# Optimization experiments

Hardware: AMD Instinct MI355X
Metric: run time of the kernel (lower is better)

Reference implementation:

```python
import jax, jax.numpy as jnp
import numpy as np

B, N, L, ND = 512, 4096, 128, 1


def setup_inputs() -> dict:
    key = jax.random.key(0)
    ks = jax.random.split(key, 20)
    g = lambda k, shape, s=0.05: jax.random.normal(k, shape, dtype=jnp.float32) * s
    IN = 3 * L + ND  # MLP input: [mem, mem, delta_t, x]
    inp = {
        "x": jax.random.normal(ks[0], (B, N, ND), jnp.float32),
        "memory": jax.random.normal(ks[1], (N, L), jnp.float32),
        "delta_t": jax.random.normal(ks[2], (B, N, L), jnp.float32),
        "src_w1": g(ks[3], (L, IN)), "src_b1": g(ks[4], (L,)),
        "src_w2": g(ks[5], (L, L)), "src_b2": g(ks[6], (L,)),
        "tar_w1": g(ks[7], (L, IN)), "tar_b1": g(ks[8], (L,)),
        "tar_w2": g(ks[9], (L, L)), "tar_b2": g(ks[10], (L,)),
        "gru_wih": g(ks[11], (3 * L, L)), "gru_whh": g(ks[12], (3 * L, L)),
        "gru_bih": g(ks[13], (3 * L,)), "gru_bhh": g(ks[14], (3 * L,)),
        "source": jax.random.randint(ks[15], (B, 1), 0, N, dtype=jnp.int64),
        "target": jax.random.randint(ks[16], (B, 1), 0, N, dtype=jnp.int64),
    }
    return inp


def _mlp(h, w1, b1, w2, b2):
    return jax.nn.relu(h @ w1.T + b1) @ w2.T + b2


def _gru_cell(inp, h, wih, whh, bih, bhh):
    gi = inp @ wih.T + bih          # [n, 3L]
    gh = h @ whh.T + bhh            # [n, 3L]
    i_r, i_z, i_n = jnp.split(gi, 3, axis=-1)
    h_r, h_z, h_n = jnp.split(gh, 3, axis=-1)
    r = jax.nn.sigmoid(i_r + h_r)
    z = jax.nn.sigmoid(i_z + h_z)
    n = jnp.tanh(i_n + r * h_n)
    return (1.0 - z) * n + z * h


def reference(x, memory, delta_t, src_w1, src_b1, src_w2, src_b2,
              tar_w1, tar_b1, tar_w2, tar_b2,
              gru_wih, gru_whh, gru_bih, gru_bhh, source, target):
    b = x.shape[0]
    bi = jnp.arange(b)
    s = source[:, 0]
    t = target[:, 0]
    src_mem = memory[s]                 # [B, L]
    tar_mem = memory[t]                 # [B, L]
    src_x = x[bi, s, :]                 # [B, ND]
    tar_x = x[bi, t, :]
    src_dt = delta_t[bi, s, :]          # [B, L]
    tar_dt = delta_t[bi, t, :]
    src_in = jnp.concatenate([src_mem, tar_mem, src_dt, src_x], axis=-1)
    tar_in = jnp.concatenate([tar_mem, src_mem, tar_dt, tar_x], axis=-1)
    src_msg = _mlp(src_in, src_w1, src_b1, src_w2, src_b2)
    tar_msg = _mlp(tar_in, tar_w1, tar_b1, tar_w2, tar_b2)

    # unique + scatter_mean == segment-mean over node ids, touching only seen nodes
    ids = jnp.concatenate([s, t], axis=0)                       # [2B]
    msgs = jnp.concatenate([src_msg, tar_msg], axis=0)          # [2B, L]
    n_nodes = memory.shape[0]
    msg_sum = jax.ops.segment_sum(msgs, ids, num_segments=n_nodes)
    cnt = jax.ops.segment_sum(jnp.ones((ids.shape[0],), msgs.dtype), ids,
                              num_segments=n_nodes)
    agg = msg_sum / jnp.maximum(cnt, 1.0)[:, None]              # [N, L]
    new_mem = _gru_cell(agg, memory, gru_wih, gru_whh, gru_bih, gru_bhh)
    seen = (cnt > 0)[:, None]
    return jnp.where(seen, new_mem, memory)
```

## Files before the change

kernel.cpp:

```cpp
#include <hip/hip_runtime.h>
#include <math.h>

#define BB 512
#define NN 4096
#define LL 128
#define IN_DIM 385
#define NK4_1 97
#define NK4_2 32
#define EPB 2
#define GPB 4

#define OFF_MSG   0
#define OFF_CNT   (OFF_MSG + NN * LL)
#define OFF_COUNT (OFF_CNT + NN)
#define OFF_LIST  (OFF_COUNT + 4)
#define OFF_W1PS  529416
#define OFF_W1PT  (OFF_W1PS + NK4_1 * LL * 4)
#define OFF_W2PS  (OFF_W1PT + NK4_1 * LL * 4)
#define OFF_W2PT  (OFF_W2PS + NK4_2 * LL * 4)
#define OFF_WIHP  (OFF_W2PT + NK4_2 * LL * 4)
#define OFF_WHHP  (OFF_WIHP + 3 * NK4_2 * LL * 4)

__global__ __launch_bounds__(256) void prep_kernel(
    const float* __restrict__ sw1, const float* __restrict__ tw1,
    const float* __restrict__ sw2, const float* __restrict__ tw2,
    const float* __restrict__ wih, const float* __restrict__ whh,
    float* __restrict__ ws)
{
    const int i = blockIdx.x * 256 + threadIdx.x;
    const int stride = gridDim.x * 256;

    float4* msg4 = (float4*)(ws + OFF_MSG);
    const float4 z4 = make_float4(0.f, 0.f, 0.f, 0.f);
    for (int idx = i; idx < NN * LL / 4; idx += stride)
        msg4[idx] = z4;
    for (int idx = i; idx < NN; idx += stride)
        ws[OFF_CNT + idx] = 0.0f;
    if (i == 0)
        ((int*)ws)[OFF_COUNT] = 0;

    float4* w1ps = (float4*)(ws + OFF_W1PS);
    float4* w1pt = (float4*)(ws + OFF_W1PT);
    for (int idx = i; idx < NK4_1 * LL; idx += stride) {
        const int k4 = idx >> 7, j = idx & 127;
        const int k = k4 * 4;
        float4 a, b;
        a.x = sw1[j * IN_DIM + k];     b.x = tw1[j * IN_DIM + k];
        a.y = (k + 1 < IN_DIM) ? sw1[j * IN_DIM + k + 1] : 0.f;
        b.y = (k + 1 < IN_DIM) ? tw1[j * IN_DIM + k + 1] : 0.f;
        a.z = (k + 2 < IN_DIM) ? sw1[j * IN_DIM + k + 2] : 0.f;
        b.z = (k + 2 < IN_DIM) ? tw1[j * IN_DIM + k + 2] : 0.f;
        a.w = (k + 3 < IN_DIM) ? sw1[j * IN_DIM + k + 3] : 0.f;
        b.w = (k + 3 < IN_DIM) ? tw1[j * IN_DIM + k + 3] : 0.f;
        w1ps[idx] = a; w1pt[idx] = b;
    }
    float4* w2ps = (float4*)(ws + OFF_W2PS);
    float4* w2pt = (float4*)(ws + OFF_W2PT);
    for (int idx = i; idx < NK4_2 * LL; idx += stride) {
        const int k4 = idx >> 7, j = idx & 127;
        const int k = k4 * 4;
        w2ps[idx] = make_float4(sw2[j * LL + k], sw2[j * LL + k + 1],
                                sw2[j * LL + k + 2], sw2[j * LL + k + 3]);
        w2pt[idx] = make_float4(tw2[j * LL + k], tw2[j * LL + k + 1],
                                tw2[j * LL + k + 2], tw2[j * LL + k + 3]);
    }
    float4* wihp = (float4*)(ws + OFF_WIHP);
    float4* whhp = (float4*)(ws + OFF_WHHP);
    for (int idx = i; idx < 3 * NK4_2 * LL; idx += stride) {
        const int j = idx & 127;
        const int gk = idx >> 7;
        const int gate = gk >> 5, k4 = gk & 31;
        const int row = gate * LL + j, k = k4 * 4;
        wihp[idx] = make_float4(wih[row * LL + k], wih[row * LL + k + 1],
                                wih[row * LL + k + 2], wih[row * LL + k + 3]);
        whhp[idx] = make_float4(whh[row * LL + k], whh[row * LL + k + 1],
                                whh[row * LL + k + 2], whh[row * LL + k + 3]);
    }
}

__global__ __launch_bounds__(256) void edge_msg_kernel(
    const float* __restrict__ x,
    const float* __restrict__ memory,
    const float* __restrict__ delta_t,
    const float* __restrict__ sb1, const float* __restrict__ sb2,
    const float* __restrict__ tb1, const float* __restrict__ tb2,
    const int* __restrict__ source, const int* __restrict__ target,
    float* __restrict__ ws, float* __restrict__ out)
{
    const int tid = threadIdx.x;

    if (blockIdx.x >= 512) {
        const int cb = blockIdx.x - 512;
        float4* out4 = (float4*)out;
        const float4* mem4 = (const float4*)memory;
        for (int idx = cb * 256 + tid; idx < NN * LL / 4; idx += 32 * 256)
            out4[idx] = mem4[idx];
        return;
    }

    const int side  = blockIdx.x & 1;
    const int chunk = blockIdx.x >> 1;
    const int g     = tid >> 7;
    const int j     = tid & 127;

    const int eg0 = chunk * EPB, eg1 = eg0 + 1;
    const int s0 = source[eg0], t0 = target[eg0];
    const int s1 = source[eg1], t1 = target[eg1];
    const int node0  = side ? t0 : s0, other0 = side ? s0 : t0;
    const int node1  = side ? t1 : s1, other1 = side ? s1 : t1;

    __shared__ float h1[LL][EPB];
    __shared__ float part1[2][EPB][LL];
    __shared__ float part2[2][EPB][LL];

    const float4* w1p = (const float4*)(ws + (side ? OFF_W1PT : OFF_W1PS));
    const float4* w2p = (const float4*)(ws + (side ? OFF_W2PT : OFF_W2PS));
    const float* b1  = side ? tb1 : sb1;
    const float* b2  = side ? tb2 : sb2;

    {
        float a0 = 0.f, a1 = 0.f;
        const float* dA = delta_t + ((size_t)eg0 * NN + node0) * LL;
        const float* dB = delta_t + ((size_t)eg1 * NN + node1) * LL;
        if (g == 0) {
            const float* pA = memory + (size_t)node0 * LL;
            const float* pB = memory + (size_t)node1 * LL;
            #pragma unroll 4
            for (int k4 = 0; k4 < 32; ++k4) {
                const float4 w  = w1p[k4 * LL + j];
                const float4 iA = *(const float4*)(pA + 4 * k4);
                const float4 iB = *(const float4*)(pB + 4 * k4);
                a0 = fmaf(w.x, iA.x, a0); a1 = fmaf(w.x, iB.x, a1);
                a0 = fmaf(w.y, iA.y, a0); a1 = fmaf(w.y, iB.y, a1);
                a0 = fmaf(w.z, iA.z, a0); a1 = fmaf(w.z, iB.z, a1);
                a0 = fmaf(w.w, iA.w, a0); a1 = fmaf(w.w, iB.w, a1);
            }
            #pragma unroll 4
            for (int k4 = 64; k4 < 80; ++k4) {
                const float4 w  = w1p[k4 * LL + j];
                const float4 iA = *(const float4*)(dA + 4 * (k4 - 64));
                const float4 iB = *(const float4*)(dB + 4 * (k4 - 64));
                a0 = fmaf(w.x, iA.x, a0); a1 = fmaf(w.x, iB.x, a1);
                a0 = fmaf(w.y, iA.y, a0); a1 = fmaf(w.y, iB.y, a1);
                a0 = fmaf(w.z, iA.z, a0); a1 = fmaf(w.z, iB.z, a1);
                a0 = fmaf(w.w, iA.w, a0); a1 = fmaf(w.w, iB.w, a1);
            }
        } else {
            const float* pA = memory + (size_t)other0 * LL;
            const float* pB = memory + (size_t)other1 * LL;
            #pragma unroll 4
            for (int k4 = 32; k4 < 64; ++k4) {
                const float4 w  = w1p[k4 * LL + j];
                const float4 iA = *(const float4*)(pA + 4 * (k4 - 32));
                const float4 iB = *(const float4*)(pB + 4 * (k4 - 32));
                a0 = fmaf(w.x, iA.x, a0); a1 = fmaf(w.x, iB.x, a1);
                a0 = fmaf(w.y, iA.y, a0); a1 = fmaf(w.y, iB.y, a1);
                a0 = fmaf(w.z, iA.z, a0); a1 = fmaf(w.z, iB.z, a1);
                a0 = fmaf(w.w, iA.w, a0); a1 = fmaf(w.w, iB.w, a1);
            }
            #pragma unroll 4
            for (int k4 = 80; k4 < 96; ++k4) {
                const float4 w  = w1p[k4 * LL + j];
                const float4 iA = *(const float4*)(dA + 4 * (k4 - 64));
                const float4 iB = *(const float4*)(dB + 4 * (k4 - 64));
                a0 = fmaf(w.x, iA.x, a0); a1 = fmaf(w.x, iB.x, a1);
                a0 = fmaf(w.y, iA.y, a0); a1 = fmaf(w.y, iB.y, a1);
                a0 = fmaf(w.z, iA.z, a0); a1 = fmaf(w.z, iB.z, a1);
                a0 = fmaf(w.w, iA.w, a0); a1 = fmaf(w.w, iB.w, a1);
            }
            {
                const float4 w = w1p[96 * LL + j];
                const float xA = x[(size_t)eg0 * NN + node0];
                const float xB = x[(size_t)eg1 * NN + node1];
                a0 = fmaf(w.x, xA, a0);
                a1 = fmaf(w.x, xB, a1);
            }
        }
        part1[g][0][j] = a0;
        part1[g][1][j] = a1;
    }
    __syncthreads();

    h1[j][g] = fmaxf(part1[0][g][j] + part1[1][g][j] + b1[j], 0.0f);
    __syncthreads();

    {
        const int k40 = g * 16, k41 = k40 + 16;
        float a0 = 0.f, a1 = 0.f;
        #pragma unroll 4
        for (int k4 = k40; k4 < k41; ++k4) {
            const float4 w  = w2p[k4 * LL + j];
            const float4 h0 = *(const float4*)&h1[k4 * 4][0];
            const float4 h2 = *(const float4*)&h1[k4 * 4 + 2][0];
            a0 = fmaf(w.x, h0.x, a0); a1 = fmaf(w.x, h0.y, a1);
            a0 = fmaf(w.y, h0.z, a0); a1 = fmaf(w.y, h0.w, a1);
            a0 = fmaf(w.z, h2.x, a0); a1 = fmaf(w.z, h2.y, a1);
            a0 = fmaf(w.w, h2.z, a0); a1 = fmaf(w.w, h2.w, a1);
        }
        part2[g][0][j] = a0;
        part2[g][1][j] = a1;
    }
    __syncthreads();

    {
        const int node = g ? node1 : node0;
        const float m = part2[0][g][j] + part2[1][g][j] + b2[j];
        atomicAdd(ws + OFF_MSG + (size_t)node * LL + j, m);
    }
    if (tid < EPB) {
        const int node = tid ? node1 : node0;
        const float old = atomicAdd(ws + OFF_CNT + node, 1.0f);
        if (old == 0.0f) {
            const int pos = atomicAdd((int*)ws + OFF_COUNT, 1);
            ((int*)ws)[OFF_LIST + pos] = node;
        }
    }
}

__global__ __launch_bounds__(256) void gru_kernel(
    const float* __restrict__ memory,
    const float* __restrict__ bih, const float* __restrict__ bhh,
    const float* __restrict__ ws,
    float* __restrict__ out)
{
    const int tid = threadIdx.x;
    const int g = tid >> 7, j = tid & 127;
    const int scount = ((const int*)ws)[OFF_COUNT];
    const int base = blockIdx.x * GPB;
    if (base >= scount) return;
    const int nact = min(GPB, scount - base);

    __shared__ float gates[6][GPB][LL];
    __shared__ int   nodes_sh[GPB];

    int nd[GPB];
    #pragma unroll
    for (int s = 0; s < GPB; ++s)
        nd[s] = (base + s < scount) ? ((const int*)ws)[OFF_LIST + base + s]
                                    : ((const int*)ws)[OFF_LIST + base];
    if (tid < GPB) nodes_sh[tid] = nd[tid];

    const float* op0; const float* op1; const float* op2; const float* op3;
    float rc0 = 1.f, rc1 = 1.f, rc2 = 1.f, rc3 = 1.f;
    if (g == 0) {
        op0 = ws + OFF_MSG + (size_t)nd[0] * LL;
        op1 = ws + OFF_MSG + (size_t)nd[1] * LL;
        op2 = ws + OFF_MSG + (size_t)nd[2] * LL;
        op3 = ws + OFF_MSG + (size_t)nd[3] * LL;
        rc0 = 1.0f / ws[OFF_CNT + nd[0]];
        rc1 = 1.0f / ws[OFF_CNT + nd[1]];
        rc2 = 1.0f / ws[OFF_CNT + nd[2]];
        rc3 = 1.0f / ws[OFF_CNT + nd[3]];
    } else {
        op0 = memory + (size_t)nd[0] * LL;
        op1 = memory + (size_t)nd[1] * LL;
        op2 = memory + (size_t)nd[2] * LL;
        op3 = memory + (size_t)nd[3] * LL;
    }

    const float4* wp = (const float4*)(ws + (g ? OFF_WHHP : OFF_WIHP));
    float a0[GPB] = {}, a1[GPB] = {}, a2[GPB] = {};
    #pragma unroll 2
    for (int k4 = 0; k4 < NK4_2; ++k4) {
        const float4 w0 = wp[(0 * NK4_2 + k4) * LL + j];
        const float4 w1 = wp[(1 * NK4_2 + k4) * LL + j];
        const float4 w2 = wp[(2 * NK4_2 + k4) * LL + j];
        const float4 v0 = *(const float4*)(op0 + 4 * k4);
        const float4 v1 = *(const float4*)(op1 + 4 * k4);
        const float4 v2 = *(const float4*)(op2 + 4 * k4);
        const float4 v3 = *(const float4*)(op3 + 4 * k4);
        a0[0] = fmaf(w0.x, v0.x, a0[0]); a0[0] = fmaf(w0.y, v0.y, a0[0]);
        a0[0] = fmaf(w0.z, v0.z, a0[0]); a0[0] = fmaf(w0.w, v0.w, a0[0]);
        a1[0] = fmaf(w1.x, v0.x, a1[0]); a1[0] = fmaf(w1.y, v0.y, a1[0]);
        a1[0] = fmaf(w1.z, v0.z, a1[0]); a1[0] = fmaf(w1.w, v0.w, a1[0]);
        a2[0] = fmaf(w2.x, v0.x, a2[0]); a2[0] = fmaf(w2.y, v0.y, a2[0]);
        a2[0] = fmaf(w2.z, v0.z, a2[0]); a2[0] = fmaf(w2.w, v0.w, a2[0]);

        a0[1] = fmaf(w0.x, v1.x, a0[1]); a0[1] = fmaf(w0.y, v1.y, a0[1]);
        a0[1] = fmaf(w0.z, v1.z, a0[1]); a0[1] = fmaf(w0.w, v1.w, a0[1]);
        a1[1] = fmaf(w1.x, v1.x, a1[1]); a1[1] = fmaf(w1.y, v1.y, a1[1]);
        a1[1] = fmaf(w1.z, v1.z, a1[1]); a1[1] = fmaf(w1.w, v1.w, a1[1]);
        a2[1] = fmaf(w2.x, v1.x, a2[1]); a2[1] = fmaf(w2.y, v1.y, a2[1]);
        a2[1] = fmaf(w2.z, v1.z, a2[1]); a2[1] = fmaf(w2.w, v1.w, a2[1]);

        a0[2] = fmaf(w0.x, v2.x, a0[2]); a0[2] = fmaf(w0.y, v2.y, a0[2]);
        a0[2] = fmaf(w0.z, v2.z, a0[2]); a0[2] = fmaf(w0.w, v2.w, a0[2]);
        a1[2] = fmaf(w1.x, v2.x, a1[2]); a1[2] = fmaf(w1.y, v2.y, a1[2]);
        a1[2] = fmaf(w1.z, v2.z, a1[2]); a1[2] = fmaf(w1.w, v2.w, a1[2]);
        a2[2] = fmaf(w2.x, v2.x, a2[2]); a2[2] = fmaf(w2.y, v2.y, a2[2]);
        a2[2] = fmaf(w2.z, v2.z, a2[2]); a2[2] = fmaf(w2.w, v2.w, a2[2]);

        a0[3] = fmaf(w0.x, v3.x, a0[3]); a0[3] = fmaf(w0.y, v3.y, a0[3]);
        a0[3] = fmaf(w0.z, v3.z, a0[3]); a0[3] = fmaf(w0.w, v3.w, a0[3]);
        a1[3] = fmaf(w1.x, v3.x, a1[3]); a1[3] = fmaf(w1.y, v3.y, a1[3]);
        a1[3] = fmaf(w1.z, v3.z, a1[3]); a1[3] = fmaf(w1.w, v3.w, a1[3]);
        a2[3] = fmaf(w2.x, v3.x, a2[3]); a2[3] = fmaf(w2.y, v3.y, a2[3]);
        a2[3] = fmaf(w2.z, v3.z, a2[3]); a2[3] = fmaf(w2.w, v3.w, a2[3]);
    }
    if (g == 0) {
        a0[0] *= rc0; a1[0] *= rc0; a2[0] *= rc0;
        a0[1] *= rc1; a1[1] *= rc1; a2[1] *= rc1;
        a0[2] *= rc2; a1[2] *= rc2; a2[2] *= rc2;
        a0[3] *= rc3; a1[3] *= rc3; a2[3] *= rc3;
    }
    #pragma unroll
    for (int s = 0; s < GPB; ++s) {
        gates[g * 3 + 0][s][j] = a0[s];
        gates[g * 3 + 1][s][j] = a1[s];
        gates[g * 3 + 2][s][j] = a2[s];
    }
    __syncthreads();

    const int total = nact * LL;
    for (int o = tid; o < total; o += 256) {
        const int s = o >> 7, jj = o & 127;
        const int node = nodes_sh[s];
        const float ir = gates[0][s][jj] + bih[jj];
        const float iz = gates[1][s][jj] + bih[LL + jj];
        const float inn = gates[2][s][jj] + bih[2 * LL + jj];
        const float hr = gates[3][s][jj] + bhh[jj];
        const float hz = gates[4][s][jj] + bhh[LL + jj];
        const float hn = gates[5][s][jj] + bhh[2 * LL + jj];
        const float r = 1.0f / (1.0f + __expf(-(ir + hr)));
        const float z = 1.0f / (1.0f + __expf(-(iz + hz)));
        const float n = tanhf(inn + r * hn);
        const float h = memory[(size_t)node * LL + jj];
        out[(size_t)node * LL + jj] = (1.0f - z) * n + z * h;
    }
}

extern "C" void kernel_launch(void* const* d_in, const int* in_sizes, int n_in,
                              void* d_out, int out_size, void* d_ws, size_t ws_size,
                              hipStream_t stream) {
    const float* x        = (const float*)d_in[0];
    const float* memory   = (const float*)d_in[1];
    const float* delta_t  = (const float*)d_in[2];
    const float* src_w1   = (const float*)d_in[3];
    const float* src_b1   = (const float*)d_in[4];
    const float* src_w2   = (const float*)d_in[5];
    const float* src_b2   = (const float*)d_in[6];
    const float* tar_w1   = (const float*)d_in[7];
    const float* tar_b1   = (const float*)d_in[8];
    const float* tar_w2   = (const float*)d_in[9];
    const float* tar_b2   = (const float*)d_in[10];
    const float* gru_wih  = (const float*)d_in[11];
    const float* gru_whh  = (const float*)d_in[12];
    const float* gru_bih  = (const float*)d_in[13];
    const float* gru_bhh  = (const float*)d_in[14];
    const int*   source   = (const int*)d_in[15];
    const int*   target   = (const int*)d_in[16];

    float* out = (float*)d_out;
    float* ws  = (float*)d_ws;

    prep_kernel<<<512, 256, 0, stream>>>(
        src_w1, tar_w1, src_w2, tar_w2, gru_wih, gru_whh, ws);

    edge_msg_kernel<<<544, 256, 0, stream>>>(
        x, memory, delta_t, src_b1, src_b2, tar_b1, tar_b2,
        source, target, ws, out);

    gru_kernel<<<1024 / GPB, 256, 0, stream>>>(
        memory, gru_bih, gru_bhh, ws, out);
}
```

Baseline: 35.68 us.

## Fuse edge-message and GRU kernels with a software grid barrier

Merges the edge MLP/scatter kernel and the GRU kernel into one persistent launch of 512 blocks. The phases are separated by a global atomic counter barrier with spin-sleep. After the barrier, each block copies only the unseen memory rows and runs the GRU for two active nodes, staging inputs in shared memory. This removes one kernel launch and the full memory-to-out copy, but it relies on all 512 blocks being co-resident and adds barrier latency.

```diff
diff --git a/kernel.cpp b/kernel.cpp
--- a/kernel.cpp
+++ b/kernel.cpp
@@ -8,18 +8,21 @@
 #define NK4_1 97
 #define NK4_2 32
 #define EPB 2
-#define GPB 4
+#define NBLK 512
 
 #define OFF_MSG   0
 #define OFF_CNT   (OFF_MSG + NN * LL)
 #define OFF_COUNT (OFF_CNT + NN)
 #define OFF_LIST  (OFF_COUNT + 4)
-#define OFF_W1PS  529416
+#define OFF_DONE  (OFF_LIST + 1024)
+#define OFF_W1PS  (OFF_DONE + 4)
 #define OFF_W1PT  (OFF_W1PS + NK4_1 * LL * 4)
 #define OFF_W2PS  (OFF_W1PT + NK4_1 * LL * 4)
 #define OFF_W2PT  (OFF_W2PS + NK4_2 * LL * 4)
 #define OFF_WIHP  (OFF_W2PT + NK4_2 * LL * 4)
 #define OFF_WHHP  (OFF_WIHP + 3 * NK4_2 * LL * 4)
+
+#define AGENT __HIP_MEMORY_SCOPE_AGENT
 
 __global__ __launch_bounds__(256) void prep_kernel(
     const float* __restrict__ sw1, const float* __restrict__ tw1,
@@ -36,8 +39,10 @@
         msg4[idx] = z4;
     for (int idx = i; idx < NN; idx += stride)
         ws[OFF_CNT + idx] = 0.0f;
-    if (i == 0)
+    if (i == 0) {
         ((int*)ws)[OFF_COUNT] = 0;
+        ((int*)ws)[OFF_DONE] = 0;
+    }
 
     float4* w1ps = (float4*)(ws + OFF_W1PS);
     float4* w1pt = (float4*)(ws + OFF_W1PT);
@@ -78,254 +83,238 @@
     }
 }
 
-__global__ __launch_bounds__(256) void edge_msg_kernel(
+__global__ __launch_bounds__(256) void fused_kernel(
     const float* __restrict__ x,
     const float* __restrict__ memory,
     const float* __restrict__ delta_t,
     const float* __restrict__ sb1, const float* __restrict__ sb2,
     const float* __restrict__ tb1, const float* __restrict__ tb2,
+    const float* __restrict__ bih, const float* __restrict__ bhh,
     const int* __restrict__ source, const int* __restrict__ target,
     float* __restrict__ ws, float* __restrict__ out)
 {
     const int tid = threadIdx.x;
-
-    if (blockIdx.x >= 512) {
-        const int cb = blockIdx.x - 512;
-        float4* out4 = (float4*)out;
-        const float4* mem4 = (const float4*)memory;
-        for (int idx = cb * 256 + tid; idx < NN * LL / 4; idx += 32 * 256)
-            out4[idx] = mem4[idx];
-        return;
-    }
-
-    const int side  = blockIdx.x & 1;
-    const int chunk = blockIdx.x >> 1;
-    const int g     = tid >> 7;
-    const int j     = tid & 127;
-
+    const int bid = blockIdx.x;
+    const int g   = tid >> 7;
+    const int j   = tid & 127;
+
+    __shared__ float h1[LL][EPB];
+    __shared__ float part1[2][EPB][LL];
+    __shared__ float part2[2][EPB][LL];
+
+    const int side  = bid & 1;
+    const int chunk = bid >> 1;
     const int eg0 = chunk * EPB, eg1 = eg0 + 1;
     const int s0 = source[eg0], t0 = target[eg0];
     const int s1 = source[eg1], t1 = target[eg1];
     const int node0  = side ? t0 : s0, other0 = side ? s0 : t0;
     const int node1  = side ? t1 : s1, other1 = side ? s1 : t1;
 
-    __shared__ float h1[LL][EPB];
-    __shared__ float part1[2][EPB][LL];
-    __shared__ float part2[2][EPB][LL];
-
-    const float4* w1p = (const float4*)(ws + (side ? OFF_W1PT : OFF_W1PS));
-    const float4* w2p = (const float4*)(ws + (side ? OFF_W2PT : OFF_W2PS));
-    const float* b1  = side ? tb1 : sb1;
-    const float* b2  = side ? tb2 : sb2;
-
     {
-        float a0 = 0.f, a1 = 0.f;
-        const float* dA = delta_t + ((size_t)eg0 * NN + node0) * LL;
-        const float* dB = delta_t + ((size_t)eg1 * NN + node1) * LL;
+        const float4* w1p = (const float4*)(ws + (side ? OFF_W1PT : OFF_W1PS));
+        const float4* w2p = (const float4*)(ws + (side ? OFF_W2PT : OFF_W2PS));
+        const float* b1  = side ? tb1 : sb1;
+        const float* b2  = side ? tb2 : sb2;
+
+        {
+            float a0 = 0.f, a1 = 0.f;
+            const float* dA = delta_t + ((size_t)eg0 * NN + node0) * LL;
+            const float* dB = delta_t + ((size_t)eg1 * NN + node1) * LL;
+            if (g == 0) {
+                const float* pA = memory + (size_t)node0 * LL;
+                const float* pB = memory + (size_t)node1 * LL;
+                #pragma unroll 4
+                for (int k4 = 0; k4 < 32; ++k4) {
+                    const float4 w  = w1p[k4 * LL + j];
+                    const float4 iA = *(const float4*)(pA + 4 * k4);
+                    const float4 iB = *(const float4*)(pB + 4 * k4);
+                    a0 = fmaf(w.x, iA.x, a0); a1 = fmaf(w.x, iB.x, a1);
+                    a0 = fmaf(w.y, iA.y, a0); a1 = fmaf(w.y, iB.y, a1);
+                    a0 = fmaf(w.z, iA.z, a0); a1 = fmaf(w.z, iB.z, a1);
+                    a0 = fmaf(w.w, iA.w, a0); a1 = fmaf(w.w, iB.w, a1);
+                }
+                #pragma unroll 4
+                for (int k4 = 64; k4 < 80; ++k4) {
+                    const float4 w  = w1p[k4 * LL + j];
+                    const float4 iA = *(const float4*)(dA + 4 * (k4 - 64));
+                    const float4 iB = *(const float4*)(dB + 4 * (k4 - 64));
+                    a0 = fmaf(w.x, iA.x, a0); a1 = fmaf(w.x, iB.x, a1);
+                    a0 = fmaf(w.y, iA.y, a0); a1 = fmaf(w.y, iB.y, a1);
+                    a0 = fmaf(w.z, iA.z, a0); a1 = fmaf(w.z, iB.z, a1);
+                    a0 = fmaf(w.w, iA.w, a0); a1 = fmaf(w.w, iB.w, a1);
+                }
+            } else {
+                const float* pA = memory + (size_t)other0 * LL;
+                const float* pB = memory + (size_t)other1 * LL;
+                #pragma unroll 4
+                for (int k4 = 32; k4 < 64; ++k4) {
+                    const float4 w  = w1p[k4 * LL + j];
+                    const float4 iA = *(const float4*)(pA + 4 * (k4 - 32));
+                    const float4 iB = *(const float4*)(pB + 4 * (k4 - 32));
+                    a0 = fmaf(w.x, iA.x, a0); a1 = fmaf(w.x, iB.x, a1);
+                    a0 = fmaf(w.y, iA.y, a0); a1 = fmaf(w.y, iB.y, a1);
+                    a0 = fmaf(w.z, iA.z, a0); a1 = fmaf(w.z, iB.z, a1);
+                    a0 = fmaf(w.w, iA.w, a0); a1 = fmaf(w.w, iB.w, a1);
+                }
+                #pragma unroll 4
+                for (int k4 = 80; k4 < 96; ++k4) {
+                    const float4 w  = w1p[k4 * LL + j];
+                    const float4 iA = *(const float4*)(dA + 4 * (k4 - 64));
+                    const float4 iB = *(const float4*)(dB + 4 * (k4 - 64));
+                    a0 = fmaf(w.x, iA.x, a0); a1 = fmaf(w.x, iB.x, a1);
+                    a0 = fmaf(w.y, iA.y, a0); a1 = fmaf(w.y, iB.y, a1);
+                    a0 = fmaf(w.z, iA.z, a0); a1 = fmaf(w.z, iB.z, a1);
+                    a0 = fmaf(w.w, iA.w, a0); a1 = fmaf(w.w, iB.w, a1);
+                }
+                {
+                    const float4 w = w1p[96 * LL + j];
+                    a0 = fmaf(w.x, x[(size_t)eg0 * NN + node0], a0);
+                    a1 = fmaf(w.x, x[(size_t)eg1 * NN + node1], a1);
+                }
+            }
+            part1[g][0][j] = a0;
+            part1[g][1][j] = a1;
+        }
+        __syncthreads();
+
+        h1[j][g] = fmaxf(part1[0][g][j] + part1[1][g][j] + b1[j], 0.0f);
+        __syncthreads();
+
+        {
+            const int k40 = g * 16, k41 = k40 + 16;
+            float a0 = 0.f, a1 = 0.f;
+            #pragma unroll 4
+            for (int k4 = k40; k4 < k41; ++k4) {
+                const float4 w  = w2p[k4 * LL + j];
+                const float4 h0 = *(const float4*)&h1[k4 * 4][0];
+                const float4 h2 = *(const float4*)&h1[k4 * 4 + 2][0];
+                a0 = fmaf(w.x, h0.x, a0); a1 = fmaf(w.x, h0.y, a1);
+                a0 = fmaf(w.y, h0.z, a0); a1 = fmaf(w.y, h0.w, a1);
+                a0 = fmaf(w.z, h2.x, a0); a1 = fmaf(w.z, h2.y, a1);
+                a0 = fmaf(w.w, h2.z, a0); a1 = fmaf(w.w, h2.w, a1);
+            }
+            part2[g][0][j] = a0;
+            part2[g][1][j] = a1;
+        }
+        __syncthreads();
+
+        {
+            const int node = g ? node1 : node0;
+            const float m = part2[0][g][j] + part2[1][g][j] + b2[j];
+            atomicAdd(ws + OFF_MSG + (size_t)node * LL + j, m);
+        }
+        if (tid < EPB) {
+            const int node = tid ? node1 : node0;
+            const float old = atomicAdd(ws + OFF_CNT + node, 1.0f);
+            if (old == 0.0f) {
+                const int pos = atomicAdd((int*)ws + OFF_COUNT, 1);
+                ((int*)ws)[OFF_LIST + pos] = node;
+            }
+        }
+    }
+
+    __syncthreads();
+    if (tid == 0) {
+        __threadfence();
+        atomicAdd((int*)ws + OFF_DONE, 1);
+        while (__hip_atomic_load((int*)ws + OFF_DONE, __ATOMIC_ACQUIRE, AGENT)
+               < NBLK)
+            __builtin_amdgcn_s_sleep(1);
+    }
+    __syncthreads();
+
+    {
+        const int node = bid * 8 + (tid >> 5);
+        const int f4i  = tid & 31;
+        const float c = __hip_atomic_load(ws + OFF_CNT + node,
+                                          __ATOMIC_RELAXED, AGENT);
+        if (c == 0.0f)
+            ((float4*)out)[(size_t)node * 32 + f4i] =
+                ((const float4*)memory)[(size_t)node * 32 + f4i];
+    }
+
+    {
+        const int scount = __hip_atomic_load((const int*)ws + OFF_COUNT,
+                                             __ATOMIC_RELAXED, AGENT);
+        const int base = bid * 2;
+        if (base >= scount) return;
+        const int nact = min(2, scount - base);
+
+        __shared__ float ah[LL][4];
+        __shared__ float gates[6][2][LL];
+        __shared__ int   nodes_sh[2];
+
+        int nd[2];
+        nd[0] = __hip_atomic_load((const int*)ws + OFF_LIST + base,
+                                  __ATOMIC_RELAXED, AGENT);
+        nd[1] = (nact > 1)
+              ? __hip_atomic_load((const int*)ws + OFF_LIST + base + 1,
+                                  __ATOMIC_RELAXED, AGENT)
+              : nd[0];
+        if (tid < 2) nodes_sh[tid] = nd[tid];
+
         if (g == 0) {
-            const float* pA = memory + (size_t)node0 * LL;
-            const float* pB = memory + (size_t)node1 * LL;
-            #pragma unroll 4
-            for (int k4 = 0; k4 < 32; ++k4) {
-                const float4 w  = w1p[k4 * LL + j];
-                const float4 iA = *(const float4*)(pA + 4 * k4);
-                const float4 iB = *(const float4*)(pB + 4 * k4);
-                a0 = fmaf(w.x, iA.x, a0); a1 = fmaf(w.x, iB.x, a1);
-                a0 = fmaf(w.y, iA.y, a0); a1 = fmaf(w.y, iB.y, a1);
-                a0 = fmaf(w.z, iA.z, a0); a1 = fmaf(w.z, iB.z, a1);
-                a0 = fmaf(w.w, iA.w, a0); a1 = fmaf(w.w, iB.w, a1);
-            }
-            #pragma unroll 4
-            for (int k4 = 64; k4 < 80; ++k4) {
-                const float4 w  = w1p[k4 * LL + j];
-                const float4 iA = *(const float4*)(dA + 4 * (k4 - 64));
-                const float4 iB = *(const float4*)(dB + 4 * (k4 - 64));
-                a0 = fmaf(w.x, iA.x, a0); a1 = fmaf(w.x, iB.x, a1);
-                a0 = fmaf(w.y, iA.y, a0); a1 = fmaf(w.y, iB.y, a1);
-                a0 = fmaf(w.z, iA.z, a0); a1 = fmaf(w.z, iB.z, a1);
-                a0 = fmaf(w.w, iA.w, a0); a1 = fmaf(w.w, iB.w, a1);
+            #pragma unroll
+            for (int s = 0; s < 2; ++s) {
+                const float c = __hip_atomic_load(ws + OFF_CNT + nd[s],
+                                                  __ATOMIC_RELAXED, AGENT);
+                const float m = __hip_atomic_load(
+                    ws + OFF_MSG + (size_t)nd[s] * LL + j,
+                    __ATOMIC_RELAXED, AGENT);
+                ah[j][s] = m / c;
             }
         } else {
-            const float* pA = memory + (size_t)other0 * LL;
-            const float* pB = memory + (size_t)other1 * LL;
-            #pragma unroll 4
-            for (int k4 = 32; k4 < 64; ++k4) {
-                const float4 w  = w1p[k4 * LL + j];
-                const float4 iA = *(const float4*)(pA + 4 * (k4 - 32));
-                const float4 iB = *(const float4*)(pB + 4 * (k4 - 32));
-                a0 = fmaf(w.x, iA.x, a0); a1 = fmaf(w.x, iB.x, a1);
-                a0 = fmaf(w.y, iA.y, a0); a1 = fmaf(w.y, iB.y, a1);
-                a0 = fmaf(w.z, iA.z, a0); a1 = fmaf(w.z, iB.z, a1);
-                a0 = fmaf(w.w, iA.w, a0); a1 = fmaf(w.w, iB.w, a1);
-            }
-            #pragma unroll 4
-            for (int k4 = 80; k4 < 96; ++k4) {
-                const float4 w  = w1p[k4 * LL + j];
-                const float4 iA = *(const float4*)(dA + 4 * (k4 - 64));
-                const float4 iB = *(const float4*)(dB + 4 * (k4 - 64));
-                a0 = fmaf(w.x, iA.x, a0); a1 = fmaf(w.x, iB.x, a1);
-                a0 = fmaf(w.y, iA.y, a0); a1 = fmaf(w.y, iB.y, a1);
-                a0 = fmaf(w.z, iA.z, a0); a1 = fmaf(w.z, iB.z, a1);
-                a0 = fmaf(w.w, iA.w, a0); a1 = fmaf(w.w, iB.w, a1);
-            }
-            {
-                const float4 w = w1p[96 * LL + j];
-                const float xA = x[(size_t)eg0 * NN + node0];
-                const float xB = x[(size_t)eg1 * NN + node1];
-                a0 = fmaf(w.x, xA, a0);
-                a1 = fmaf(w.x, xB, a1);
-            }
-        }
-        part1[g][0][j] = a0;
-        part1[g][1][j] = a1;
-    }
-    __syncthreads();
-
-    h1[j][g] = fmaxf(part1[0][g][j] + part1[1][g][j] + b1[j], 0.0f);
-    __syncthreads();
-
-    {
-        const int k40 = g * 16, k41 = k40 + 16;
-        float a0 = 0.f, a1 = 0.f;
-        #pragma unroll 4
-        for (int k4 = k40; k4 < k41; ++k4) {
-            const float4 w  = w2p[k4 * LL + j];
-            const float4 h0 = *(const float4*)&h1[k4 * 4][0];
-            const float4 h2 = *(const float4*)&h1[k4 * 4 + 2][0];
-            a0 = fmaf(w.x, h0.x, a0); a1 = fmaf(w.x, h0.y, a1);
-            a0 = fmaf(w.y, h0.z, a0); a1 = fmaf(w.y, h0.w, a1);
-            a0 = fmaf(w.z, h2.x, a0); a1 = fmaf(w.z, h2.y, a1);
-            a0 = fmaf(w.w, h2.z, a0); a1 = fmaf(w.w, h2.w, a1);
-        }
-        part2[g][0][j] = a0;
-        part2[g][1][j] = a1;
-    }
-    __syncthreads();
-
-    {
-        const int node = g ? node1 : node0;
-        const float m = part2[0][g][j] + part2[1][g][j] + b2[j];
-        atomicAdd(ws + OFF_MSG + (size_t)node * LL + j, m);
-    }
-    if (tid < EPB) {
-        const int node = tid ? node1 : node0;
-        const float old = atomicAdd(ws + OFF_CNT + node, 1.0f);
-        if (old == 0.0f) {
-            const int pos = atomicAdd((int*)ws + OFF_COUNT, 1);
-            ((int*)ws)[OFF_LIST + pos] = node;
-        }
-    }
-}
-
-__global__ __launch_bounds__(256) void gru_kernel(
-    const float* __restrict__ memory,
-    const float* __restrict__ bih, const float* __restrict__ bhh,
-    const float* __restrict__ ws,
-    float* __restrict__ out)
-{
-    const int tid = threadIdx.x;
-    const int g = tid >> 7, j = tid & 127;
-    const int scount = ((const int*)ws)[OFF_COUNT];
-    const int base = blockIdx.x * GPB;
-    if (base >= scount) return;
-    const int nact = min(GPB, scount - base);
-
-    __shared__ float gates[6][GPB][LL];
-    __shared__ int   nodes_sh[GPB];
-
-    int nd[GPB];
-    #pragma unroll
-    for (int s = 0; s < GPB; ++s)
-        nd[s] = (base + s < scount) ? ((const int*)ws)[OFF_LIST + base + s]
-                                    : ((const int*)ws)[OFF_LIST + base];
-    if (tid < GPB) nodes_sh[tid] = nd[tid];
-
-    const float* op0; const float* op1; const float* op2; const float* op3;
-    float rc0 = 1.f, rc1 = 1.f, rc2 = 1.f, rc3 = 1.f;
-    if (g == 0) {
-        op0 = ws + OFF_MSG + (size_t)nd[0] * LL;
-        op1 = ws + OFF_MSG + (size_t)nd[1] * LL;
-        op2 = ws + OFF_MSG + (size_t)nd[2] * LL;
-        op3 = ws + OFF_MSG + (size_t)nd[3] * LL;
-        rc0 = 1.0f / ws[OFF_CNT + nd[0]];
-        rc1 = 1.0f / ws[OFF_CNT + nd[1]];
-        rc2 = 1.0f / ws[OFF_CNT + nd[2]];
-        rc3 = 1.0f / ws[OFF_CNT + nd[3]];
-    } else {
-        op0 = memory + (size_t)nd[0] * LL;
-        op1 = memory + (size_t)nd[1] * LL;
-        op2 = memory + (size_t)nd[2] * LL;
-        op3 = memory + (size_t)nd[3] * LL;
-    }
-
-    const float4* wp = (const float4*)(ws + (g ? OFF_WHHP : OFF_WIHP));
-    float a0[GPB] = {}, a1[GPB] = {}, a2[GPB] = {};
-    #pragma unroll 2
-    for (int k4 = 0; k4 < NK4_2; ++k4) {
-        const float4 w0 = wp[(0 * NK4_2 + k4) * LL + j];
-        const float4 w1 = wp[(1 * NK4_2 + k4) * LL + j];
-        const float4 w2 = wp[(2 * NK4_2 + k4) * LL + j];
-        const float4 v0 = *(const float4*)(op0 + 4 * k4);
-        const float4 v1 = *(const float4*)(op1 + 4 * k4);
-        const float4 v2 = *(const float4*)(op2 + 4 * k4);
-        const float4 v3 = *(const float4*)(op3 + 4 * k4);
-        a0[0] = fmaf(w0.x, v0.x, a0[0]); a0[0] = fmaf(w0.y, v0.y, a0[0]);
-        a0[0] = fmaf(w0.z, v0.z, a0[0]); a0[0] = fmaf(w0.w, v0.w, a0[0]);
-        a1[0] = fmaf(w1.x, v0.x, a1[0]); a1[0] = fmaf(w1.y, v0.y, a1[0]);
-        a1[0] = fmaf(w1.z, v0.z, a1[0]); a1[0] = fmaf(w1.w, v0.w, a1[0]);
-        a2[0] = fmaf(w2.x, v0.x, a2[0]); a2[0] = fmaf(w2.y, v0.y, a2[0]);
-        a2[0] = fmaf(w2.z, v0.z, a2[0]); a2[0] = fmaf(w2.w, v0.w, a2[0]);
-
-        a0[1] = fmaf(w0.x, v1.x, a0[1]); a0[1] = fmaf(w0.y, v1.y, a0[1]);
-        a0[1] = fmaf(w0.z, v1.z, a0[1]); a0[1] = fmaf(w0.w, v1.w, a0[1]);
-        a1[1] = fmaf(w1.x, v1.x, a1[1]); a1[1] = fmaf(w1.y, v1.y, a1[1]);
-        a1[1] = fmaf(w1.z, v1.z, a1[1]); a1[1] = fmaf(w1.w, v1.w, a1[1]);
-        a2[1] = fmaf(w2.x, v1.x, a2[1]); a2[1] = fmaf(w2.y, v1.y, a2[1]);
-        a2[1] = fmaf(w2.z, v1.z, a2[1]); a2[1] = fmaf(w2.w, v1.w, a2[1]);
-
-        a0[2] = fmaf(w0.x, v2.x, a0[2]); a0[2] = fmaf(w0.y, v2.y, a0[2]);
-        a0[2] = fmaf(w0.z, v2.z, a0[2]); a0[2] = fmaf(w0.w, v2.w, a0[2]);
-        a1[2] = fmaf(w1.x, v2.x, a1[2]); a1[2] = fmaf(w1.y, v2.y, a1[2]);
-        a1[2] = fmaf(w1.z, v2.z, a1[2]); a1[2] = fmaf(w1.w, v2.w, a1[2]);
-        a2[2] = fmaf(w2.x, v2.x, a2[2]); a2[2] = fmaf(w2.y, v2.y, a2[2]);
-        a2[2] = fmaf(w2.z, v2.z, a2[2]); a2[2] = fmaf(w2.w, v2.w, a2[2]);
-
-        a0[3] = fmaf(w0.x, v3.x, a0[3]); a0[3] = fmaf(w0.y, v3.y, a0[3]);
-        a0[3] = fmaf(w0.z, v3.z, a0[3]); a0[3] = fmaf(w0.w, v3.w, a0[3]);
-        a1[3] = fmaf(w1.x, v3.x, a1[3]); a1[3] = fmaf(w1.y, v3.y, a1[3]);
-        a1[3] = fmaf(w1.z, v3.z, a1[3]); a1[3] = fmaf(w1.w, v3.w, a1[3]);
-        a2[3] = fmaf(w2.x, v3.x, a2[3]); a2[3] = fmaf(w2.y, v3.y, a2[3]);
-        a2[3] = fmaf(w2.z, v3.z, a2[3]); a2[3] = fmaf(w2.w, v3.w, a2[3]);
-    }
-    if (g == 0) {
-        a0[0] *= rc0; a1[0] *= rc0; a2[0] *= rc0;
-        a0[1] *= rc1; a1[1] *= rc1; a2[1] *= rc1;
-        a0[2] *= rc2; a1[2] *= rc2; a2[2] *= rc2;
-        a0[3] *= rc3; a1[3] *= rc3; a2[3] *= rc3;
-    }
-    #pragma unroll
-    for (int s = 0; s < GPB; ++s) {
-        gates[g * 3 + 0][s][j] = a0[s];
-        gates[g * 3 + 1][s][j] = a1[s];
-        gates[g * 3 + 2][s][j] = a2[s];
-    }
-    __syncthreads();
-
-    const int total = nact * LL;
-    for (int o = tid; o < total; o += 256) {
-        const int s = o >> 7, jj = o & 127;
-        const int node = nodes_sh[s];
-        const float ir = gates[0][s][jj] + bih[jj];
-        const float iz = gates[1][s][jj] + bih[LL + jj];
-        const float inn = gates[2][s][jj] + bih[2 * LL + jj];
-        const float hr = gates[3][s][jj] + bhh[jj];
-        const float hz = gates[4][s][jj] + bhh[LL + jj];
-        const float hn = gates[5][s][jj] + bhh[2 * LL + jj];
-        const float r = 1.0f / (1.0f + __expf(-(ir + hr)));
-        const float z = 1.0f / (1.0f + __expf(-(iz + hz)));
-        const float n = tanhf(inn + r * hn);
-        const float h = memory[(size_t)node * LL + jj];
-        out[(size_t)node * LL + jj] = (1.0f - z) * n + z * h;
+            #pragma unroll
+            for (int s = 0; s < 2; ++s)
+                ah[j][2 + s] = memory[(size_t)nd[s] * LL + j];
+        }
+        __syncthreads();
+
+        const float4* wp = (const float4*)(ws + (g ? OFF_WHHP : OFF_WIHP));
+        float a0[2] = {}, a1[2] = {}, a2[2] = {};
+        #pragma unroll 2
+        for (int k4 = 0; k4 < NK4_2; ++k4) {
+            const float4 w0 = wp[(0 * NK4_2 + k4) * LL + j];
+            const float4 w1 = wp[(1 * NK4_2 + k4) * LL + j];
+            const float4 w2 = wp[(2 * NK4_2 + k4) * LL + j];
+            const float w0a[4] = {w0.x, w0.y, w0.z, w0.w};
+            const float w1a[4] = {w1.x, w1.y, w1.z, w1.w};
+            const float w2a[4] = {w2.x, w2.y, w2.z, w2.w};
+            #pragma unroll
+            for (int c = 0; c < 4; ++c) {
+                const float2 v2 = *(const float2*)&ah[k4 * 4 + c][g * 2];
+                a0[0] = fmaf(w0a[c], v2.x, a0[0]);
+                a1[0] = fmaf(w1a[c], v2.x, a1[0]);
+                a2[0] = fmaf(w2a[c], v2.x, a2[0]);
+                a0[1] = fmaf(w0a[c], v2.y, a0[1]);
+                a1[1] = fmaf(w1a[c], v2.y, a1[1]);
+                a2[1] = fmaf(w2a[c], v2.y, a2[1]);
+            }
+        }
+        #pragma unroll
+        for (int s = 0; s < 2; ++s) {
+            gates[g * 3 + 0][s][j] = a0[s];
+            gates[g * 3 + 1][s][j] = a1[s];
+            gates[g * 3 + 2][s][j] = a2[s];
+        }
+        __syncthreads();
+
+        const int total = nact * LL;
+        for (int o = tid; o < total; o += 256) {
+            const int s = o >> 7, jj = o & 127;
+            const int node = nodes_sh[s];
+            const float ir = gates[0][s][jj] + bih[jj];
+            const float iz = gates[1][s][jj] + bih[LL + jj];
+            const float inn = gates[2][s][jj] + bih[2 * LL + jj];
+            const float hr = gates[3][s][jj] + bhh[jj];
+            const float hz = gates[4][s][jj] + bhh[LL + jj];
+            const float hn = gates[5][s][jj] + bhh[2 * LL + jj];
+            const float r = 1.0f / (1.0f + __expf(-(ir + hr)));
+            const float z = 1.0f / (1.0f + __expf(-(iz + hz)));
+            const float n = tanhf(inn + r * hn);
+            const float h = memory[(size_t)node * LL + jj];
+            out[(size_t)node * LL + jj] = (1.0f - z) * n + z * h;
+        }
     }
 }
 
@@ -356,10 +345,7 @@
     prep_kernel<<<512, 256, 0, stream>>>(
         src_w1, tar_w1, src_w2, tar_w2, gru_wih, gru_whh, ws);
 
-    edge_msg_kernel<<<544, 256, 0, stream>>>(
+    fused_kernel<<<NBLK, 256, 0, stream>>>(
         x, memory, delta_t, src_b1, src_b2, tar_b1, tar_b2,
-        source, target, ws, out);
-
-    gru_kernel<<<1024 / GPB, 256, 0, stream>>>(
-        memory, gru_bih, gru_bhh, ws, out);
+        gru_bih, gru_bhh, source, target, ws, out);
 }
```

After: 63.97 us. 1.79x slower.
